# Optimization experiments

Measured on AMD Instinct MI355X. Metric: run time of the kernel, lower is better.

## Reference

```python
import jax, jax.numpy as jnp
import numpy as np

# dims matching init_kwargs
B, S, D, DH, E, K = 16, 8192, 256, 512, 8, 2


def setup_inputs() -> dict:
    key = jax.random.key(0)
    k0, k1, k2, k3 = jax.random.split(key, 4)
    scale = 0.02
    x = jax.random.normal(k0, (B, S, D), dtype=jnp.float32)
    gate_w = jax.random.normal(k1, (E, D), dtype=jnp.float32) * scale   # Linear(d_model, E, bias=False): weight [E, D]
    w1 = jax.random.normal(k2, (E, DH, D), dtype=jnp.float32) * scale   # fc1 weight per expert [DH, D]
    b1 = jnp.zeros((E, DH), dtype=jnp.float32)
    w2 = jax.random.normal(k3, (E, D, DH), dtype=jnp.float32) * scale   # fc2 weight per expert [D, DH]
    b2 = jnp.zeros((E, D), dtype=jnp.float32)
    return {"x": x, "gate_w": gate_w, "w1": w1, "b1": b1, "w2": w2, "b2": b2}


def reference(x, gate_w, w1, b1, w2, b2):
    b, s, d = x.shape
    e = gate_w.shape[0]
    xf = x.reshape(-1, d)                      # [T, D]
    T = xf.shape[0]

    # --- TopKRouter ---
    logits = xf @ gate_w.T                     # [T, E]
    probs = jax.nn.softmax(logits, axis=-1)
    topk_p, topk_i = jax.lax.top_k(probs, K)   # [T, K]
    topk_w = topk_p / topk_p.sum(axis=-1, keepdims=True)
    # load-balancing aux loss
    sel_mask = jax.nn.one_hot(topk_i, e, dtype=jnp.float32).sum(axis=1)  # [T, E]
    f_i = sel_mask.mean(axis=0)
    p_i = probs.mean(axis=0)
    aux_loss = e * jnp.sum(f_i * p_i)

    # --- dispatch: dense per-token expert weights (0 for unselected) ---
    dense_w = jnp.zeros((T, e), dtype=x.dtype).at[
        jnp.arange(T)[:, None], topk_i
    ].add(topk_w)                              # [T, E]

    # --- experts: loop over small fixed E; weight is zero for unselected tokens,
    # so this computes the same math as the sparse gather/scatter loop ---
    out = jnp.zeros_like(xf)
    for ei in range(e):
        h = jax.nn.silu(xf @ w1[ei].T + b1[ei])     # [T, DH]
        y = h @ w2[ei].T + b2[ei]                   # [T, D]
        out = out + dense_w[:, ei:ei + 1] * y

    return out.reshape(b, s, d), aux_loss
```

## Files before the change

### kernel.cpp

```cpp
#include <hip/hip_runtime.h>

typedef __attribute__((ext_vector_type(8))) short short8;
typedef __attribute__((ext_vector_type(4))) float f32x4;

#define T_TOK  131072
#define DMODEL 256
#define DHID   512
#define NEXP   8


__device__ __forceinline__ unsigned short f2bf(float f) {
  unsigned int u = __float_as_uint(f);
  u = (u + 0x7FFFu + ((u >> 16) & 1u)) >> 16;
  return (unsigned short)u;
}
__device__ __forceinline__ float bf2f(unsigned short u) {
  return __uint_as_float(((unsigned)u) << 16);
}

__device__ __forceinline__ void gload16(const void* g, void* l) {
  __builtin_amdgcn_global_load_lds(
      (const __attribute__((address_space(1))) void*)g,
      (__attribute__((address_space(3))) void*)l, 16, 0, 0);
}

__global__ void k_wconv(const float* __restrict__ w1, const float* __restrict__ w2,
                        const float* __restrict__ gate,
                        unsigned short* __restrict__ P1, unsigned short* __restrict__ P2,
                        double* __restrict__ gate_d) {
  int g = blockIdx.x * 256 + threadIdx.x;
  if (g < 2048) gate_d[g] = (double)gate[g];
  int e = g >> 14, rem = g & 16383;
  {
    int row = rem >> 5, c = rem & 31;
    int kc = c >> 3, cs = c & 7;
    const float* s = w1 + ((size_t)e * DHID + row) * DMODEL + c * 8;
    short8 v;
#pragma unroll
    for (int j = 0; j < 8; ++j) v[j] = (short)f2bf(s[j]);
    size_t dc = ((size_t)(e * 4 + kc) * 512 + row) * 8 + (cs ^ (row & 7));
    *(short8*)(P1 + dc * 8) = v;
  }
  {
    int row = rem >> 6, c = rem & 63;
    int kc = c >> 3, cs = c & 7;
    const float* s = w2 + ((size_t)e * DMODEL + row) * DHID + c * 8;
    short8 v;
#pragma unroll
    for (int j = 0; j < 8; ++j) v[j] = (short)f2bf(s[j]);
    size_t dc = ((size_t)(e * 8 + kc) * 256 + row) * 8 + (cs ^ (row & 7));
    *(short8*)(P2 + dc * 8) = v;
  }
}

__global__ __launch_bounds__(256, 2) void k_router(
    const float* __restrict__ x, const double* __restrict__ gd,
    unsigned short* __restrict__ xb, int* __restrict__ pack, float2* __restrict__ tkw,
    int* __restrict__ part_cnt, float* __restrict__ part_psum) {
  __shared__ float xs[16384];
  __shared__ double red[1024];
  __shared__ int s_cnt[NEXP];
  __shared__ float s_ps[NEXP];
  int tid = threadIdx.x;
  int tok = tid & 63, q = tid >> 6;
  int qu = __builtin_amdgcn_readfirstlane(q);

  for (int c = 0; c < 4; ++c) {
    if (tid < NEXP) { s_cnt[tid] = 0; s_ps[tid] = 0.f; }
    int tb = (blockIdx.x << 8) + (c << 6);
    __syncthreads();

#pragma unroll
    for (int i = 0; i < 16; ++i) {
      int idx = i * 256 + tid;
      int row = idx >> 6, c4 = (idx & 63) << 2;
      float4 v = *(const float4*)(x + (size_t)(tb + row) * 256 + c4);
      int sw = row & 31;
      float* xr = xs + row * 256;
      xr[(c4 + 0) ^ sw] = v.x;
      xr[(c4 + 1) ^ sw] = v.y;
      xr[(c4 + 2) ^ sw] = v.z;
      xr[(c4 + 3) ^ sw] = v.w;
      ushort4 u4;
      u4.x = f2bf(v.x); u4.y = f2bf(v.y); u4.z = f2bf(v.z); u4.w = f2bf(v.w);
      *(ushort4*)(xb + (size_t)(tb + row) * 256 + c4) = u4;
    }
    __syncthreads();

    double acc[8] = {0, 0, 0, 0, 0, 0, 0, 0};
    {
      int sw = tok & 31;
      const float* xr = xs + tok * 256;
#pragma unroll 4
      for (int d0 = 0; d0 < 64; ++d0) {
        int d = (qu << 6) + d0;
        double xv = (double)xr[d ^ sw];
#pragma unroll
        for (int e = 0; e < 8; ++e) acc[e] += xv * gd[e * 256 + d];
      }
    }

    double l[8];
#pragma unroll
    for (int j = 0; j < 4; ++j) red[tid * 4 + j] = acc[j];
    __syncthreads();
    if (tid < 64) {
#pragma unroll
      for (int j = 0; j < 4; ++j)
        l[j] = red[tid * 4 + j] + red[(64 + tid) * 4 + j] +
               red[(128 + tid) * 4 + j] + red[(192 + tid) * 4 + j];
    }
    __syncthreads();
#pragma unroll
    for (int j = 0; j < 4; ++j) red[tid * 4 + j] = acc[4 + j];
    __syncthreads();
    if (tid < 64) {
#pragma unroll
      for (int j = 0; j < 4; ++j)
        l[4 + j] = red[tid * 4 + j] + red[(64 + tid) * 4 + j] +
                   red[(128 + tid) * 4 + j] + red[(192 + tid) * 4 + j];
      int t = tb + tid;
      int i1 = 0;
#pragma unroll
      for (int e = 1; e < NEXP; ++e) if (l[e] > l[i1]) i1 = e;
      int i2 = (i1 == 0) ? 1 : 0;
#pragma unroll
      for (int e = 0; e < NEXP; ++e) if (e != i1 && l[e] > l[i2]) i2 = e;
      double m = l[0];
#pragma unroll
      for (int e = 1; e < NEXP; ++e) m = (l[e] > m) ? l[e] : m;
      float pe[NEXP]; float s = 0.f;
#pragma unroll
      for (int e = 0; e < NEXP; ++e) { pe[e] = __expf((float)(l[e] - m)); s += pe[e]; }
      float inv = 1.f / s;
      float p1 = pe[i1] * inv, p2 = pe[i2] * inv;
      float wn = 1.f / (p1 + p2);
      pack[t] = i1 | (i2 << 8);
      tkw[t] = make_float2(p1 * wn, p2 * wn);
      atomicAdd(&s_cnt[i1], 1); atomicAdd(&s_cnt[i2], 1);
#pragma unroll
      for (int e = 0; e < NEXP; ++e) atomicAdd(&s_ps[e], pe[e] * inv);
    }
    __syncthreads();
    if (tid < NEXP) {
      part_cnt[(blockIdx.x * 4 + c) * NEXP + tid] = s_cnt[tid];
      part_psum[(blockIdx.x * 4 + c) * NEXP + tid] = s_ps[tid];
    }
  }
}

__global__ __launch_bounds__(512) void k_scan(
    const int* __restrict__ part_cnt, const float* __restrict__ part_psum,
    int* __restrict__ block_off, int* __restrict__ cnt_total, float* __restrict__ out) {
  __shared__ float s_ps[NEXP];
  __shared__ int s_ct[NEXP];
  int lane = threadIdx.x & 63, wv = threadIdx.x >> 6;
  int base = lane * 32;
  int lsum = 0; float ps = 0.f;
#pragma unroll 8
  for (int j = 0; j < 32; ++j) {
    lsum += part_cnt[(base + j) * NEXP + wv];
    ps += part_psum[(base + j) * NEXP + wv];
  }
  int incl = lsum;
#pragma unroll
  for (int d = 1; d < 64; d <<= 1) { int t = __shfl_up(incl, d); if (lane >= d) incl += t; }
  int run = incl - lsum;
#pragma unroll 8
  for (int j = 0; j < 32; ++j) {
    int v = part_cnt[(base + j) * NEXP + wv];
    block_off[(base + j) * NEXP + wv] = run;
    run += v;
  }
#pragma unroll
  for (int d = 32; d; d >>= 1) ps += __shfl_xor(ps, d);
  int total = __shfl(incl, 63);
  if (lane == 0) { cnt_total[wv] = total; s_ct[wv] = total; s_ps[wv] = ps; }
  __syncthreads();
  if (threadIdx.x == 0) {
    double aux = 0.0; int rb = 0;
    for (int e = 0; e < NEXP; ++e) {
      aux += ((double)s_ct[e] / 131072.0) * ((double)s_ps[e] / 131072.0);
      cnt_total[8 + e] = rb;
      rb += (s_ct[e] + 255) & ~255;
    }
    out[33554432] = (float)(8.0 * aux);
  }
}

__global__ void k_scatter(const int* __restrict__ pack, float2* tkw,
                          const int* __restrict__ block_off, const int* __restrict__ cnt_total,
                          int* __restrict__ tok_list, float* __restrict__ wt_list) {
  __shared__ int s_loc[NEXP];
  int tid = threadIdx.x;
  if (tid < NEXP) s_loc[tid] = 0;
  __syncthreads();
  int t = (blockIdx.x << 6) + tid;
  int p = pack[t];
  float2 wv = tkw[t];
  int e1 = p & 255, e2 = (p >> 8) & 255;
  int o1 = block_off[blockIdx.x * NEXP + e1];
  int p1 = atomicAdd(&s_loc[e1], 1);
  int i1 = cnt_total[8 + e1] + o1 + p1;
  tok_list[i1] = t; wt_list[i1] = wv.x;
  int o2 = block_off[blockIdx.x * NEXP + e2];
  int p2 = atomicAdd(&s_loc[e2], 1);
  int i2 = cnt_total[8 + e2] + o2 + p2;
  tok_list[i2] = t; wt_list[i2] = wv.y;
  tkw[t] = make_float2(__int_as_float(i1), __int_as_float(i2));
}

__global__ __launch_bounds__(512, 2) void k_gemm1(
    const unsigned short* __restrict__ xb, const unsigned short* __restrict__ P1,
    const float* __restrict__ b1, const int* __restrict__ tok_list,
    const int* __restrict__ cnt_total, unsigned short* __restrict__ Hp) {
  __shared__ __align__(16) unsigned short buf[32768];
  __shared__ int s_tok[128];

  int bid = (blockIdx.x & 7) * 1029 + (blockIdx.x >> 3);
  int e = -1, loc = 0, cum = 0, cnte = 0;
#pragma unroll
  for (int ee = 0; ee < NEXP; ++ee) {
    int ct = cnt_total[ee];
    int nb = ((ct + 127) >> 7) * 4;
    if (e < 0 && bid < cum + nb) { e = ee; loc = bid - cum; cnte = ct; }
    cum += nb;
  }
  if (e < 0) return;
  int mi = loc >> 2, ni = loc & 3;
  int nv = cnte - (mi << 7); if (nv > 128) nv = 128;
  int hbp = cnt_total[8 + e];

  int tid = threadIdx.x;
  int lane = tid & 63, w = tid >> 6, l15 = lane & 15, lg = lane >> 4;
  int wr = w >> 2, wc = w & 3;

  float b1v[2];
#pragma unroll
  for (int nt = 0; nt < 2; ++nt)
    b1v[nt] = b1[e * DHID + ni * 128 + wc * 32 + nt * 16 + l15];

  if (tid < 128) s_tok[tid] = tok_list[hbp + (mi << 7) + (tid < nv ? tid : nv - 1)];
  __syncthreads();

  int arow0 = tid >> 3, acs = tid & 7;
  const unsigned short* pa[2];
#pragma unroll
  for (int i = 0; i < 2; ++i) {
    int row = i * 64 + arow0;
    pa[i] = xb + (size_t)s_tok[row] * DMODEL + ((acs ^ (row & 7)) << 3);
  }
  const unsigned short* pb = P1 + ((size_t)(e * 4) * 512 + ni * 128) * 64;

  auto stage = [&](int kc) {
    int ab = (kc & 1) * 8192, bb = 16384 + (kc & 1) * 8192;
#pragma unroll
    for (int i = 0; i < 2; ++i)
      gload16(pa[i] + kc * 64, &buf[(size_t)(ab + (i * 512 + w * 64) * 8)]);
    const unsigned short* src = pb + (size_t)kc * 32768;
#pragma unroll
    for (int i = 0; i < 2; ++i) {
      int c = i * 512 + tid;
      gload16(src + (size_t)c * 8, &buf[(size_t)(bb + (i * 512 + w * 64) * 8)]);
    }
  };

  int aidx[4][2], bidx[2][2];
#pragma unroll
  for (int mt = 0; mt < 4; ++mt) {
    int r = wr * 64 + mt * 16 + l15, r7 = r & 7;
#pragma unroll
    for (int ks = 0; ks < 2; ++ks) aidx[mt][ks] = r * 64 + (((ks * 4 + lg) ^ r7) << 3);
  }
#pragma unroll
  for (int nt = 0; nt < 2; ++nt) {
    int r = wc * 32 + nt * 16 + l15, r7 = r & 7;
#pragma unroll
    for (int ks = 0; ks < 2; ++ks) bidx[nt][ks] = r * 64 + (((ks * 4 + lg) ^ r7) << 3);
  }

  f32x4 acc[4][2];
#pragma unroll
  for (int mt = 0; mt < 4; ++mt)
#pragma unroll
    for (int nt = 0; nt < 2; ++nt) acc[mt][nt] = (f32x4){0.f, 0.f, 0.f, 0.f};

  stage(0);
  asm volatile("s_waitcnt vmcnt(0)" ::: "memory");
  __builtin_amdgcn_s_barrier();
  __builtin_amdgcn_sched_barrier(0);

  for (int s = 0; s < 4; ++s) {
    if (s < 3) stage(s + 1);
    int ab = (s & 1) * 8192, bb = 16384 + (s & 1) * 8192;
#pragma unroll
    for (int ks = 0; ks < 2; ++ks) {
      short8 a[4], b[2];
#pragma unroll
      for (int mt = 0; mt < 4; ++mt) a[mt] = *(const short8*)&buf[ab + aidx[mt][ks]];
#pragma unroll
      for (int nt = 0; nt < 2; ++nt) b[nt] = *(const short8*)&buf[bb + bidx[nt][ks]];
#pragma unroll
      for (int mt = 0; mt < 4; ++mt)
#pragma unroll
        for (int nt = 0; nt < 2; ++nt)
          acc[mt][nt] = __builtin_amdgcn_mfma_f32_16x16x32_bf16(a[mt], b[nt], acc[mt][nt], 0, 0, 0);
    }
    asm volatile("s_waitcnt vmcnt(0)" ::: "memory");
    __builtin_amdgcn_s_barrier();
    __builtin_amdgcn_sched_barrier(0);
  }

#pragma unroll
  for (int mt = 0; mt < 4; ++mt) {
    int rbase0 = (wr * 64 + mt * 16) * 128;
#pragma unroll
    for (int nt = 0; nt < 2; ++nt) {
      int col = wc * 32 + nt * 16 + l15;
      int c3 = col >> 3, c7 = col & 7;
#pragma unroll
      for (int rr = 0; rr < 4; ++rr) {
        int lr = lg * 4 + rr;
        int r7 = lr & 7;
        int p = (c3 & 8) | ((c3 & 7) ^ r7);
        float z = acc[mt][nt][rr] + b1v[nt];
        float sv = z * __builtin_amdgcn_rcpf(1.f + __expf(-z));
        buf[rbase0 + lr * 128 + (p << 3) + c7] =
            (unsigned short)(__float_as_uint(sv) >> 16);
      }
    }
  }
  __syncthreads();
  {
    int blk = (hbp >> 8) + (mi >> 1);
    int rbase = (mi & 1) * 128;
    short8 z8 = {0, 0, 0, 0, 0, 0, 0, 0};
#pragma unroll
    for (int i = 0; i < 4; ++i) {
      int t = i * 512 + tid;
      int row = t >> 4, s = t & 15;
      short8 v = (row < nv) ? *(const short8*)&buf[row * 128 + s * 8] : z8;
      size_t dc = ((size_t)(blk * 8 + ni * 2 + (s >> 3)) * 256 + rbase + row) * 8 + (s & 7);
      *(short8*)&Hp[dc * 8] = v;
    }
  }
}

__global__ __launch_bounds__(512, 2) void k_gemm2c(
    unsigned short* Hp, const unsigned short* __restrict__ P2,
    const float* __restrict__ b2, const float* __restrict__ wt_list,
    const int* __restrict__ cnt_total) {
  __shared__ __align__(16) unsigned short buf[65536];
  __shared__ float s_wt[256];

  int bid = (blockIdx.x & 7) * 129 + (blockIdx.x >> 3);
  int e = -1, mi = 0, cum = 0, cnte = 0;
#pragma unroll
  for (int ee = 0; ee < NEXP; ++ee) {
    int ct = cnt_total[ee];
    int nb = (ct + 255) >> 8;
    if (e < 0 && bid < cum + nb) { e = ee; mi = bid - cum; cnte = ct; }
    cum += nb;
  }
  if (e < 0) return;
  int nv = cnte - (mi << 8); if (nv > 256) nv = 256;
  int hbp = cnt_total[8 + e];
  int blk = (hbp >> 8) + mi;

  int tid = threadIdx.x;
  int lane = tid & 63, w = tid >> 6, l15 = lane & 15, lg = lane >> 4;
  int wr = w >> 2, wc = w & 3;

  float b2v[4];
#pragma unroll
  for (int nt = 0; nt < 4; ++nt)
    b2v[nt] = b2[e * DMODEL + wc * 64 + nt * 16 + l15];

  if (tid < 256) s_wt[tid] = (tid < nv) ? wt_list[hbp + (mi << 8) + tid] : 0.f;
  __syncthreads();

  auto stage = [&](int s) {
    int d = (s & 1) * 32768;
    const unsigned short* sa = Hp + (size_t)(blk * 8 + s) * 16384;
    const unsigned short* sb = P2 + (size_t)(e * 8 + s) * 16384;
#pragma unroll
    for (int i = 0; i < 4; ++i) {
      int c = i * 512 + tid;
      gload16(sa + (size_t)c * 8, &buf[d + (i * 512 + w * 64) * 8]);
    }
#pragma unroll
    for (int i = 0; i < 4; ++i) {
      int c = i * 512 + tid;
      gload16(sb + (size_t)c * 8, &buf[d + 16384 + (i * 512 + w * 64) * 8]);
    }
  };

  int aidx[8][2], bidx[4][2];
#pragma unroll
  for (int mt = 0; mt < 8; ++mt) {
    int r = wr * 128 + mt * 16 + l15, r7 = r & 7;
#pragma unroll
    for (int ks = 0; ks < 2; ++ks) aidx[mt][ks] = r * 64 + (((ks * 4 + lg) ^ r7) << 3);
  }
#pragma unroll
  for (int nt = 0; nt < 4; ++nt) {
    int r = wc * 64 + nt * 16 + l15, r7 = r & 7;
#pragma unroll
    for (int ks = 0; ks < 2; ++ks) bidx[nt][ks] = r * 64 + (((ks * 4 + lg) ^ r7) << 3);
  }

  f32x4 acc[8][4];
#pragma unroll
  for (int mt = 0; mt < 8; ++mt)
#pragma unroll
    for (int nt = 0; nt < 4; ++nt) acc[mt][nt] = (f32x4){0.f, 0.f, 0.f, 0.f};

  stage(0);
  asm volatile("s_waitcnt vmcnt(0)" ::: "memory");
  __builtin_amdgcn_s_barrier();
  __builtin_amdgcn_sched_barrier(0);

  for (int s = 0; s < 8; ++s) {
    if (s < 7) stage(s + 1);
    int ab = (s & 1) * 32768, bb = ab + 16384;
#pragma unroll
    for (int ks = 0; ks < 2; ++ks) {
      short8 a[8], b[4];
#pragma unroll
      for (int mt = 0; mt < 8; ++mt) a[mt] = *(const short8*)&buf[ab + aidx[mt][ks]];
#pragma unroll
      for (int nt = 0; nt < 4; ++nt) b[nt] = *(const short8*)&buf[bb + bidx[nt][ks]];
#pragma unroll
      for (int mt = 0; mt < 8; ++mt)
#pragma unroll
        for (int nt = 0; nt < 4; ++nt)
          acc[mt][nt] = __builtin_amdgcn_mfma_f32_16x16x32_bf16(a[mt], b[nt], acc[mt][nt], 0, 0, 0);
    }
    asm volatile("s_waitcnt vmcnt(0)" ::: "memory");
    __builtin_amdgcn_s_barrier();
    __builtin_amdgcn_sched_barrier(0);
  }

#pragma unroll
  for (int mt = 0; mt < 8; ++mt) {
    int rbase0 = (wr * 128 + mt * 16) * 256;
#pragma unroll
    for (int nt = 0; nt < 4; ++nt) {
      int col = wc * 64 + nt * 16 + l15;
#pragma unroll
      for (int rr = 0; rr < 4; ++rr) {
        int row = wr * 128 + mt * 16 + lg * 4 + rr;
        float v = s_wt[row] * (acc[mt][nt][rr] + b2v[nt]);
        buf[rbase0 + (lg * 4 + rr) * 256 + col] =
            (unsigned short)(__float_as_uint(v) >> 16);
      }
    }
  }
  __syncthreads();
  unsigned short* ydst = Hp + (size_t)blk * 131072;
#pragma unroll
  for (int i = 0; i < 16; ++i) {
    size_t cidx = (size_t)(i * 512 + tid) * 8;
    *(short8*)&ydst[cidx] = *(const short8*)&buf[cidx];
  }
}

__global__ __launch_bounds__(256) void k_reduce(
    const unsigned short* __restrict__ Y, const float2* __restrict__ inv,
    float* __restrict__ out) {
  int g = blockIdx.x * 256 + threadIdx.x;
#pragma unroll
  for (int it = 0; it < 8; ++it) {
    int t = g >> 5;
    int cw = (g & 31) << 3;
    float2 iv = inv[t];
    int s1 = __float_as_int(iv.x), s2 = __float_as_int(iv.y);
    const unsigned short* y1 = Y + (size_t)(s1 >> 8) * 131072 + (size_t)(s1 & 255) * 256 + cw;
    const unsigned short* y2 = Y + (size_t)(s2 >> 8) * 131072 + (size_t)(s2 & 255) * 256 + cw;
    short8 a = *(const short8*)y1;
    short8 b = *(const short8*)y2;
    float* op = out + (size_t)t * 256 + cw;
    float4 r0, r1;
    r0.x = bf2f((unsigned short)a[0]) + bf2f((unsigned short)b[0]);
    r0.y = bf2f((unsigned short)a[1]) + bf2f((unsigned short)b[1]);
    r0.z = bf2f((unsigned short)a[2]) + bf2f((unsigned short)b[2]);
    r0.w = bf2f((unsigned short)a[3]) + bf2f((unsigned short)b[3]);
    r1.x = bf2f((unsigned short)a[4]) + bf2f((unsigned short)b[4]);
    r1.y = bf2f((unsigned short)a[5]) + bf2f((unsigned short)b[5]);
    r1.z = bf2f((unsigned short)a[6]) + bf2f((unsigned short)b[6]);
    r1.w = bf2f((unsigned short)a[7]) + bf2f((unsigned short)b[7]);
    *(float4*)op = r0;
    *(float4*)(op + 4) = r1;
    g += 2048 * 256;
  }
}

extern "C" void kernel_launch(void* const* d_in, const int* in_sizes, int n_in,
                              void* d_out, int out_size, void* d_ws, size_t ws_size,
                              hipStream_t stream) {
  const float* x    = (const float*)d_in[0];
  const float* gate = (const float*)d_in[1];
  const float* w1   = (const float*)d_in[2];
  const float* b1   = (const float*)d_in[3];
  const float* w2   = (const float*)d_in[4];
  const float* b2   = (const float*)d_in[5];
  float* out = (float*)d_out;
  char* ws = (char*)d_ws;

  unsigned short* xb  = (unsigned short*)(ws);
  unsigned short* P1  = (unsigned short*)(ws + 67108864);
  unsigned short* P2  = (unsigned short*)(ws + 69206016);
  int*    tok_list  = (int*)(ws + 71303168);
  float*  wt_list   = (float*)(ws + 72368128);
  int*    pack      = (int*)(ws + 73433088);
  float2* tkw       = (float2*)(ws + 73957376);
  int*    part_cnt  = (int*)(ws + 75005952);
  float*  part_psum = (float*)(ws + 75071488);
  int*    block_off = (int*)(ws + 75137024);
  int*    cnt_total = (int*)(ws + 75202560);
  double* gate_d    = (double*)(ws + 75235328);
  unsigned short* Hp = (unsigned short*)(ws + 75497472);

  k_wconv<<<512, 256, 0, stream>>>(w1, w2, gate, P1, P2, gate_d);
  k_router<<<512, 256, 0, stream>>>(x, gate_d, xb, pack, tkw, part_cnt, part_psum);
  k_scan<<<1, 512, 0, stream>>>(part_cnt, part_psum, block_off, cnt_total, out);
  k_scatter<<<2048, 64, 0, stream>>>(pack, tkw, block_off, cnt_total, tok_list, wt_list);
  k_gemm1<<<8232, 512, 0, stream>>>(xb, P1, b1, tok_list, cnt_total, Hp);
  k_gemm2c<<<1032, 512, 0, stream>>>(Hp, P2, b2, wt_list, cnt_total);
  k_reduce<<<2048, 256, 0, stream>>>(Hp, tkw, out);
}
```

Baseline: 484.4 us.

## Halve gemm2 LDS footprint with 32-wide K stages and split epilogue

The packed layouts of W2 and of the hidden activations change from 64-wide to 32-wide K chunks with a 4-way XOR swizzle. This lets the second expert GEMM use 16 smaller double-buffered stages and a 64 KB shared buffer instead of 128 KB. The epilogue writes its output tile in two halves so it fits the smaller buffer. The aim is to let more blocks fit per CU and hide latency better. The cost is twice as many barriers and waits per block, fewer MFMAs between syncs, and an extra sync phase in the epilogue.

```diff
diff --git a/kernel.cpp b/kernel.cpp
--- a/kernel.cpp
+++ b/kernel.cpp
@@ -43,12 +43,12 @@
   }
   {
     int row = rem >> 6, c = rem & 63;
-    int kc = c >> 3, cs = c & 7;
+    int sg = c >> 2, cs = c & 3;
     const float* s = w2 + ((size_t)e * DMODEL + row) * DHID + c * 8;
     short8 v;
 #pragma unroll
     for (int j = 0; j < 8; ++j) v[j] = (short)f2bf(s[j]);
-    size_t dc = ((size_t)(e * 8 + kc) * 256 + row) * 8 + (cs ^ (row & 7));
+    size_t dc = ((size_t)(e * 16 + sg) * 256 + row) * 4 + (cs ^ (row & 3));
     *(short8*)(P2 + dc * 8) = v;
   }
 }
@@ -321,11 +321,11 @@
 #pragma unroll
       for (int rr = 0; rr < 4; ++rr) {
         int lr = lg * 4 + rr;
-        int r7 = lr & 7;
-        int p = (c3 & 8) | ((c3 & 7) ^ r7);
+        int r3 = lr & 3;
+        int u = (c3 & 12) | ((c3 & 3) ^ r3);
         float z = acc[mt][nt][rr] + b1v[nt];
         float sv = z * __builtin_amdgcn_rcpf(1.f + __expf(-z));
-        buf[rbase0 + lr * 128 + (p << 3) + c7] =
+        buf[rbase0 + lr * 128 + (u << 3) + c7] =
             (unsigned short)(__float_as_uint(sv) >> 16);
       }
     }
@@ -338,9 +338,9 @@
 #pragma unroll
     for (int i = 0; i < 4; ++i) {
       int t = i * 512 + tid;
-      int row = t >> 4, s = t & 15;
-      short8 v = (row < nv) ? *(const short8*)&buf[row * 128 + s * 8] : z8;
-      size_t dc = ((size_t)(blk * 8 + ni * 2 + (s >> 3)) * 256 + rbase + row) * 8 + (s & 7);
+      int row = t >> 4, u = t & 15;
+      short8 v = (row < nv) ? *(const short8*)&buf[row * 128 + u * 8] : z8;
+      size_t dc = ((size_t)(blk * 16 + ni * 4 + (u >> 2)) * 256 + rbase + row) * 4 + (u & 3);
       *(short8*)&Hp[dc * 8] = v;
     }
   }
@@ -350,7 +350,7 @@
     unsigned short* Hp, const unsigned short* __restrict__ P2,
     const float* __restrict__ b2, const float* __restrict__ wt_list,
     const int* __restrict__ cnt_total) {
-  __shared__ __align__(16) unsigned short buf[65536];
+  __shared__ __align__(16) unsigned short buf[32768];
   __shared__ float s_wt[256];
 
   int bid = (blockIdx.x & 7) * 129 + (blockIdx.x >> 3);
@@ -380,33 +380,31 @@
   __syncthreads();
 
   auto stage = [&](int s) {
-    int d = (s & 1) * 32768;
-    const unsigned short* sa = Hp + (size_t)(blk * 8 + s) * 16384;
-    const unsigned short* sb = P2 + (size_t)(e * 8 + s) * 16384;
-#pragma unroll
-    for (int i = 0; i < 4; ++i) {
+    int ab = (s & 1) * 8192, bb = 16384 + (s & 1) * 8192;
+    const unsigned short* sa = Hp + (size_t)(blk * 16 + s) * 8192;
+    const unsigned short* sb = P2 + (size_t)(e * 16 + s) * 8192;
+#pragma unroll
+    for (int i = 0; i < 2; ++i) {
       int c = i * 512 + tid;
-      gload16(sa + (size_t)c * 8, &buf[d + (i * 512 + w * 64) * 8]);
-    }
-#pragma unroll
-    for (int i = 0; i < 4; ++i) {
+      gload16(sa + (size_t)c * 8, &buf[ab + (i * 512 + w * 64) * 8]);
+    }
+#pragma unroll
+    for (int i = 0; i < 2; ++i) {
       int c = i * 512 + tid;
-      gload16(sb + (size_t)c * 8, &buf[d + 16384 + (i * 512 + w * 64) * 8]);
+      gload16(sb + (size_t)c * 8, &buf[bb + (i * 512 + w * 64) * 8]);
     }
   };
 
-  int aidx[8][2], bidx[4][2];
+  int aidx[8], bidx[4];
 #pragma unroll
   for (int mt = 0; mt < 8; ++mt) {
-    int r = wr * 128 + mt * 16 + l15, r7 = r & 7;
-#pragma unroll
-    for (int ks = 0; ks < 2; ++ks) aidx[mt][ks] = r * 64 + (((ks * 4 + lg) ^ r7) << 3);
+    int r = wr * 128 + mt * 16 + l15;
+    aidx[mt] = r * 32 + ((lg ^ (r & 3)) << 3);
   }
 #pragma unroll
   for (int nt = 0; nt < 4; ++nt) {
-    int r = wc * 64 + nt * 16 + l15, r7 = r & 7;
-#pragma unroll
-    for (int ks = 0; ks < 2; ++ks) bidx[nt][ks] = r * 64 + (((ks * 4 + lg) ^ r7) << 3);
+    int r = wc * 64 + nt * 16 + l15;
+    bidx[nt] = r * 32 + ((lg ^ (r & 3)) << 3);
   }
 
   f32x4 acc[8][4];
@@ -420,48 +418,51 @@
   __builtin_amdgcn_s_barrier();
   __builtin_amdgcn_sched_barrier(0);
 
-  for (int s = 0; s < 8; ++s) {
-    if (s < 7) stage(s + 1);
-    int ab = (s & 1) * 32768, bb = ab + 16384;
-#pragma unroll
-    for (int ks = 0; ks < 2; ++ks) {
-      short8 a[8], b[4];
-#pragma unroll
-      for (int mt = 0; mt < 8; ++mt) a[mt] = *(const short8*)&buf[ab + aidx[mt][ks]];
-#pragma unroll
-      for (int nt = 0; nt < 4; ++nt) b[nt] = *(const short8*)&buf[bb + bidx[nt][ks]];
-#pragma unroll
-      for (int mt = 0; mt < 8; ++mt)
-#pragma unroll
-        for (int nt = 0; nt < 4; ++nt)
-          acc[mt][nt] = __builtin_amdgcn_mfma_f32_16x16x32_bf16(a[mt], b[nt], acc[mt][nt], 0, 0, 0);
-    }
+  for (int s = 0; s < 16; ++s) {
+    if (s < 15) stage(s + 1);
+    int ab = (s & 1) * 8192, bb = 16384 + (s & 1) * 8192;
+    short8 a[8], b[4];
+#pragma unroll
+    for (int mt = 0; mt < 8; ++mt) a[mt] = *(const short8*)&buf[ab + aidx[mt]];
+#pragma unroll
+    for (int nt = 0; nt < 4; ++nt) b[nt] = *(const short8*)&buf[bb + bidx[nt]];
+#pragma unroll
+    for (int mt = 0; mt < 8; ++mt)
+#pragma unroll
+      for (int nt = 0; nt < 4; ++nt)
+        acc[mt][nt] = __builtin_amdgcn_mfma_f32_16x16x32_bf16(a[mt], b[nt], acc[mt][nt], 0, 0, 0);
     asm volatile("s_waitcnt vmcnt(0)" ::: "memory");
     __builtin_amdgcn_s_barrier();
     __builtin_amdgcn_sched_barrier(0);
   }
 
-#pragma unroll
-  for (int mt = 0; mt < 8; ++mt) {
-    int rbase0 = (wr * 128 + mt * 16) * 256;
-#pragma unroll
-    for (int nt = 0; nt < 4; ++nt) {
-      int col = wc * 64 + nt * 16 + l15;
-#pragma unroll
-      for (int rr = 0; rr < 4; ++rr) {
-        int row = wr * 128 + mt * 16 + lg * 4 + rr;
-        float v = s_wt[row] * (acc[mt][nt][rr] + b2v[nt]);
-        buf[rbase0 + (lg * 4 + rr) * 256 + col] =
-            (unsigned short)(__float_as_uint(v) >> 16);
+  unsigned short* ydst = Hp + (size_t)blk * 131072;
+#pragma unroll
+  for (int h = 0; h < 2; ++h) {
+    __syncthreads();
+    if (wr == h) {
+#pragma unroll
+      for (int mt = 0; mt < 8; ++mt) {
+        int rbase0 = (mt * 16) * 256;
+#pragma unroll
+        for (int nt = 0; nt < 4; ++nt) {
+          int col = wc * 64 + nt * 16 + l15;
+#pragma unroll
+          for (int rr = 0; rr < 4; ++rr) {
+            int row = h * 128 + mt * 16 + lg * 4 + rr;
+            float v = s_wt[row] * (acc[mt][nt][rr] + b2v[nt]);
+            buf[rbase0 + (lg * 4 + rr) * 256 + col] =
+                (unsigned short)(__float_as_uint(v) >> 16);
+          }
+        }
       }
     }
-  }
-  __syncthreads();
-  unsigned short* ydst = Hp + (size_t)blk * 131072;
-#pragma unroll
-  for (int i = 0; i < 16; ++i) {
-    size_t cidx = (size_t)(i * 512 + tid) * 8;
-    *(short8*)&ydst[cidx] = *(const short8*)&buf[cidx];
+    __syncthreads();
+#pragma unroll
+    for (int i = 0; i < 8; ++i) {
+      size_t cidx = (size_t)(i * 512 + tid) * 8;
+      *(short8*)&ydst[(size_t)h * 32768 + cidx] = *(const short8*)&buf[cidx];
+    }
   }
 }
 
```

New measurement: 501.3 us. 3.5% more time.
